# Performance work log

Measured on AMD Instinct MI355X. Metric: run time of the kernel, lower is better.

The kernel has to match this reference:

```python
import jax, jax.numpy as jnp
import numpy as np

S_INIT, S_FINAL = 512, 1024
LAYER_DIM, NEXT_DIM, DIM = 512, 512, 1024
BATCH = 32768


def setup_inputs() -> dict:
    rng = np.random.default_rng(0)
    # eigenvector block (trainable 'base') and its 0/1 mask
    base = np.zeros((DIM, DIM), dtype=np.float32)
    base[S_INIT:S_FINAL, S_INIT - LAYER_DIM:S_INIT] = rng.uniform(
        -0.2, 0.2, (NEXT_DIM, LAYER_DIM)).astype(np.float32)
    base_mask = np.zeros((DIM, DIM), dtype=np.float32)
    base_mask[S_INIT:S_FINAL, S_INIT - LAYER_DIM:S_INIT] = 1.0
    eye = np.eye(DIM, dtype=np.float32)
    # eigenvalue diagonal block; NOTE: trainable_diag_mask holds the *random values*
    # (not 0/1), exactly as in the original TF code.
    masks = np.zeros((DIM, DIM), dtype=np.float32)
    masks[S_INIT:S_FINAL, S_INIT:S_FINAL] = np.diag(
        rng.uniform(-1.8, 1.8, NEXT_DIM).astype(np.float32))
    untrainable_diag = eye - masks
    trainable_diag = masks.copy()
    trainable_diag_mask = masks.copy()
    # column masks selecting pass-through rows vs. activated block rows
    mask1 = np.ones((DIM, 1), dtype=np.float32)
    mask1[S_INIT:S_FINAL] = 0.0
    mask2 = np.zeros((DIM, 1), dtype=np.float32)
    mask2[S_INIT:S_FINAL] = 1.0

    key = jax.random.key(0)
    data = jax.random.normal(key, (BATCH, DIM), dtype=jnp.float32)
    return {
        "data": data,
        "base": jnp.asarray(base),
        "base_mask": jnp.asarray(base_mask),
        "eye": jnp.asarray(eye),
        "trainable_diag": jnp.asarray(trainable_diag),
        "trainable_diag_mask": jnp.asarray(trainable_diag_mask),
        "untrainable_diag": jnp.asarray(untrainable_diag),
        "mask1": jnp.asarray(mask1),
        "mask2": jnp.asarray(mask2),
    }


def reference(data, base, base_mask, eye, trainable_diag, trainable_diag_mask,
              untrainable_diag, mask1, mask2):
    # layer = masked base + I ; diag = masked trainable diag + (I - fixed diag)
    layer = base * base_mask + eye                                  # [D, D]
    diag = trainable_diag * trainable_diag_mask + untrainable_diag  # [D, D]
    x = jnp.matmul(2.0 * eye - layer, data.T)                       # [D, B]
    x = jnp.matmul(diag, x)                                         # [D, B]
    x = jnp.matmul(layer, x)                                        # [D, B]
    temp = jax.nn.relu(x)  # relu is elementwise; transpose pair cancels
    x = x * mask1 + temp * mask2                                    # [D, B]
    return x.T                                                      # [B, D]
```

## Files before the change

### kernel.cpp

```cpp
#include <hip/hip_runtime.h>


typedef float f32x4 __attribute__((ext_vector_type(4)));
typedef int   i32x4 __attribute__((ext_vector_type(4)));

#define DIMW   1024
#define HALFD  512
#define BM     128
#define BN     128
#define BK     32

__device__ __forceinline__ unsigned short f2bf(float x) {
    union { float f; unsigned int i; } c;
    c.f = x;
    unsigned int r = c.i + 0x7FFFu + ((c.i >> 16) & 1u);
    return (unsigned short)(r >> 16);
}
__device__ __forceinline__ unsigned int pack2(float a, float b) {
    return (unsigned int)f2bf(a) | ((unsigned int)f2bf(b) << 16);
}

__device__ __forceinline__ void mfma_16x16x32_bf16(f32x4& d, const i32x4& a, const i32x4& b) {
    asm volatile("v_mfma_f32_16x16x32_bf16 %0, %1, %2, %0"
                 : "+v"(d)
                 : "v"(a), "v"(b));
}
__device__ __forceinline__ void acc_fence(f32x4& d) {
    asm volatile("s_nop 7\n\ts_nop 7" : "+v"(d));
}

__global__ __launch_bounds__(256) void spectral_kernel(
    const float* __restrict__ data,
    const float* __restrict__ wsrc,
    const float* __restrict__ td,
    const float* __restrict__ tdm,
    const float* __restrict__ ud,
    float* __restrict__ out)
{
    __shared__ unsigned short As[BM * BK];
    __shared__ unsigned short Bs[BN * BK];
    __shared__ float dsh[BN];

    const int tid    = (int)threadIdx.x;
    const int lane   = tid & 63;
    const int wave   = tid >> 6;
    const int lane16 = lane & 15;
    const int quad   = lane >> 4;
    const int wm     = wave >> 1;
    const int wn     = wave & 1;
    const int rowBase = (int)blockIdx.x * BM;
    const int colBase = (int)blockIdx.y * BN;

    if (tid < BN) {
        int j = HALFD + colBase + tid;
        size_t fi = (size_t)j * DIMW + j;
        dsh[tid] = td[fi] * tdm[fi] + ud[fi];
    }

    {
        const float4* src = (const float4*)data;
        float4*       dst = (float4*)out;
        #pragma unroll
        for (int p = 0; p < 16; ++p) {
            int c  = p * 256 + tid;
            int r  = c >> 5;
            int cc = c & 31;
            size_t off = (size_t)(rowBase + r) * (DIMW / 4) + (colBase >> 2) + cc;
            dst[off] = src[off];
        }
    }

    f32x4 acc[4][4];
    #pragma unroll
    for (int mi = 0; mi < 4; ++mi)
        #pragma unroll
        for (int ni = 0; ni < 4; ++ni)
            acc[mi][ni] = (f32x4){0.f, 0.f, 0.f, 0.f};

    for (int k0 = 0; k0 < HALFD; k0 += BK) {
        float4 av[4], bv[4];
        #pragma unroll
        for (int p = 0; p < 4; ++p) {
            int c  = p * 256 + tid;
            int r  = c >> 3;
            int kc = (c & 7) * 4;
            av[p] = *(const float4*)(data + (size_t)(rowBase + r) * DIMW + k0 + kc);
            bv[p] = *(const float4*)(wsrc + (size_t)(HALFD + colBase + r) * DIMW + k0 + kc);
        }
        __syncthreads();
        #pragma unroll
        for (int p = 0; p < 4; ++p) {
            int c  = p * 256 + tid;
            int r  = c >> 3;
            int kc = (c & 7) * 4;
            uint2 ua, ub;
            ua.x = pack2(av[p].x, av[p].y);  ua.y = pack2(av[p].z, av[p].w);
            ub.x = pack2(bv[p].x, bv[p].y);  ub.y = pack2(bv[p].z, bv[p].w);
            *(uint2*)(As + r * BK + kc) = ua;
            *(uint2*)(Bs + r * BK + kc) = ub;
        }
        __syncthreads();

        i32x4 a[4], b[4];
        #pragma unroll
        for (int mi = 0; mi < 4; ++mi)
            a[mi] = *(const i32x4*)(As + (wm * 64 + mi * 16 + lane16) * BK + quad * 8);
        #pragma unroll
        for (int ni = 0; ni < 4; ++ni)
            b[ni] = *(const i32x4*)(Bs + (wn * 64 + ni * 16 + lane16) * BK + quad * 8);

        #pragma unroll
        for (int mi = 0; mi < 4; ++mi)
            #pragma unroll
            for (int ni = 0; ni < 4; ++ni)
                mfma_16x16x32_bf16(acc[mi][ni], a[mi], b[ni]);
    }

    #pragma unroll
    for (int mi = 0; mi < 4; ++mi)
        #pragma unroll
        for (int ni = 0; ni < 4; ++ni)
            acc_fence(acc[mi][ni]);

    #pragma unroll
    for (int mi = 0; mi < 4; ++mi) {
        int mBase = rowBase + wm * 64 + mi * 16 + quad * 4;
        #pragma unroll
        for (int ni = 0; ni < 4; ++ni) {
            int nloc = wn * 64 + ni * 16 + lane16;
            float dv = dsh[nloc];
            int col  = HALFD + colBase + nloc;
            #pragma unroll
            for (int r = 0; r < 4; ++r) {
                int row  = mBase + r;
                size_t gi = (size_t)row * DIMW + col;
                float u1 = data[gi];
                float v  = dv * u1 + (1.0f - dv) * acc[mi][ni][r];
                out[gi] = fmaxf(v, 0.0f);
            }
        }
    }
}

extern "C" void kernel_launch(void* const* d_in, const int* in_sizes, int n_in,
                              void* d_out, int out_size, void* d_ws, size_t ws_size,
                              hipStream_t stream) {
    const float* data = (const float*)d_in[0];
    const float* base = (const float*)d_in[1];
    const float* td   = (const float*)d_in[4];
    const float* tdm  = (const float*)d_in[5];
    const float* ud   = (const float*)d_in[6];
    float* out = (float*)d_out;

    dim3 grid(32768 / BM, HALFD / BN);
    dim3 block(256, 1, 1);
    spectral_kernel<<<grid, block, 0, stream>>>(data, base, td, tdm, ud, out);
}
```

Baseline: 302.4 us.

## Double-buffer LDS tiles with register prefetch, XOR-swizzle LDS, move passthrough copy to end

Splits the K loop into load, pack and compute stages. The next tile's global loads are issued before the MFMAs on the current tile, and two LDS buffers alternate between iterations. LDS addresses get an XOR swizzle to reduce bank conflicts on the 16-byte fragment reads. The pass-through copy of the first half of the columns moves after the epilogue, and launch bounds now request 3 blocks per SM, which may constrain register allocation. The cost is doubled LDS and held prefetch registers, with a possible risk of spills.

```diff
diff --git a/kernel.cpp b/kernel.cpp
--- a/kernel.cpp
+++ b/kernel.cpp
@@ -9,6 +9,7 @@
 #define BM     128
 #define BN     128
 #define BK     32
+#define NITER  16
 
 __device__ __forceinline__ unsigned short f2bf(float x) {
     union { float f; unsigned int i; } c;
@@ -29,7 +30,7 @@
     asm volatile("s_nop 7\n\ts_nop 7" : "+v"(d));
 }
 
-__global__ __launch_bounds__(256) void spectral_kernel(
+__global__ __launch_bounds__(256, 3) void spectral_kernel(
     const float* __restrict__ data,
     const float* __restrict__ wsrc,
     const float* __restrict__ td,
@@ -37,8 +38,8 @@
     const float* __restrict__ ud,
     float* __restrict__ out)
 {
-    __shared__ unsigned short As[BM * BK];
-    __shared__ unsigned short Bs[BN * BK];
+    __shared__ unsigned short As[2][BM * BK];
+    __shared__ unsigned short Bs[2][BN * BK];
     __shared__ float dsh[BN];
 
     const int tid    = (int)threadIdx.x;
@@ -57,19 +58,6 @@
         dsh[tid] = td[fi] * tdm[fi] + ud[fi];
     }
 
-    {
-        const float4* src = (const float4*)data;
-        float4*       dst = (float4*)out;
-        #pragma unroll
-        for (int p = 0; p < 16; ++p) {
-            int c  = p * 256 + tid;
-            int r  = c >> 5;
-            int cc = c & 31;
-            size_t off = (size_t)(rowBase + r) * (DIMW / 4) + (colBase >> 2) + cc;
-            dst[off] = src[off];
-        }
-    }
-
     f32x4 acc[4][4];
     #pragma unroll
     for (int mi = 0; mi < 4; ++mi)
@@ -77,8 +65,9 @@
         for (int ni = 0; ni < 4; ++ni)
             acc[mi][ni] = (f32x4){0.f, 0.f, 0.f, 0.f};
 
-    for (int k0 = 0; k0 < HALFD; k0 += BK) {
-        float4 av[4], bv[4];
+    float4 av[4], bv[4];
+
+    auto LOADT = [&](int k0) {
         #pragma unroll
         for (int p = 0; p < 4; ++p) {
             int c  = p * 256 + tid;
@@ -87,33 +76,54 @@
             av[p] = *(const float4*)(data + (size_t)(rowBase + r) * DIMW + k0 + kc);
             bv[p] = *(const float4*)(wsrc + (size_t)(HALFD + colBase + r) * DIMW + k0 + kc);
         }
-        __syncthreads();
+    };
+    auto PACKW = [&](int buf) {
         #pragma unroll
         for (int p = 0; p < 4; ++p) {
-            int c  = p * 256 + tid;
-            int r  = c >> 3;
-            int kc = (c & 7) * 4;
+            int c    = p * 256 + tid;
+            int r    = c >> 3;
+            int half = c & 7;
+            int idx = r * BK + ((((half >> 1) ^ ((r >> 1) & 3)) << 3)) + (half & 1) * 4;
             uint2 ua, ub;
             ua.x = pack2(av[p].x, av[p].y);  ua.y = pack2(av[p].z, av[p].w);
             ub.x = pack2(bv[p].x, bv[p].y);  ub.y = pack2(bv[p].z, bv[p].w);
-            *(uint2*)(As + r * BK + kc) = ua;
-            *(uint2*)(Bs + r * BK + kc) = ub;
+            *(uint2*)(&As[buf][idx]) = ua;
+            *(uint2*)(&Bs[buf][idx]) = ub;
         }
-        __syncthreads();
+    };
+
+    LOADT(0);
+    PACKW(0);
+    __syncthreads();
+
+    for (int it = 0; it < NITER; ++it) {
+        const int cur = it & 1;
+
+        if (it + 1 < NITER) LOADT((it + 1) * BK);
 
         i32x4 a[4], b[4];
         #pragma unroll
-        for (int mi = 0; mi < 4; ++mi)
-            a[mi] = *(const i32x4*)(As + (wm * 64 + mi * 16 + lane16) * BK + quad * 8);
+        for (int mi = 0; mi < 4; ++mi) {
+            int R = wm * 64 + mi * 16 + lane16;
+            a[mi] = *(const i32x4*)(&As[cur][R * BK + ((quad ^ ((R >> 1) & 3)) << 3)]);
+        }
         #pragma unroll
-        for (int ni = 0; ni < 4; ++ni)
-            b[ni] = *(const i32x4*)(Bs + (wn * 64 + ni * 16 + lane16) * BK + quad * 8);
+        for (int ni = 0; ni < 4; ++ni) {
+            int R = wn * 64 + ni * 16 + lane16;
+            b[ni] = *(const i32x4*)(&Bs[cur][R * BK + ((quad ^ ((R >> 1) & 3)) << 3)]);
+        }
 
         #pragma unroll
         for (int mi = 0; mi < 4; ++mi)
             #pragma unroll
             for (int ni = 0; ni < 4; ++ni)
                 mfma_16x16x32_bf16(acc[mi][ni], a[mi], b[ni]);
+
+        __syncthreads();
+        if (it + 1 < NITER) {
+            PACKW(cur ^ 1);
+            __syncthreads();
+        }
     }
 
     #pragma unroll
@@ -140,6 +150,19 @@
             }
         }
     }
+
+    {
+        const float4* src = (const float4*)data;
+        float4*       dst = (float4*)out;
+        #pragma unroll
+        for (int p = 0; p < 16; ++p) {
+            int c  = p * 256 + tid;
+            int r  = c >> 5;
+            int cc = c & 31;
+            size_t off = (size_t)(rowBase + r) * (DIMW / 4) + (colBase >> 2) + cc;
+            dst[off] = src[off];
+        }
+    }
 }
 
 extern "C" void kernel_launch(void* const* d_in, const int* in_sizes, int n_in,
```

Result: no change. 302.2 us (-0.1%).

## Keep full-K weight panel in LDS and stream A directly into registers

Applied to the files above, without the earlier changes.

Each block now holds a 64-column bf16 weight panel covering the full K range in swizzled LDS, loaded once at the start. A fragments are read from global memory straight into registers with double buffering, so the per-K-step syncthreads and the LDS staging of A are gone. Tile N shrinks to 64 with launch bounds set to 2 blocks per CU, and the pass-through copy moves after the epilogue. The cost is 64KB of LDS per block and uncoalesced 32-byte strided A loads, and the data tile is re-read by twice as many blocks.

```diff
diff --git a/kernel.cpp b/kernel.cpp
--- a/kernel.cpp
+++ b/kernel.cpp
@@ -3,12 +3,13 @@
 
 typedef float f32x4 __attribute__((ext_vector_type(4)));
 typedef int   i32x4 __attribute__((ext_vector_type(4)));
+typedef unsigned int u32x4 __attribute__((ext_vector_type(4)));
 
 #define DIMW   1024
 #define HALFD  512
 #define BM     128
-#define BN     128
-#define BK     32
+#define BN     64
+#define NITER  16
 
 __device__ __forceinline__ unsigned short f2bf(float x) {
     union { float f; unsigned int i; } c;
@@ -29,7 +30,11 @@
     asm volatile("s_nop 7\n\ts_nop 7" : "+v"(d));
 }
 
-__global__ __launch_bounds__(256) void spectral_kernel(
+__device__ __forceinline__ int bs_addr(int col, int k) {
+    return (col * 1024 + k * 2) ^ ((((col & 7) ^ ((k >> 7) & 3))) << 4);
+}
+
+__global__ __launch_bounds__(256, 2) void spectral_kernel(
     const float* __restrict__ data,
     const float* __restrict__ wsrc,
     const float* __restrict__ td,
@@ -37,9 +42,7 @@
     const float* __restrict__ ud,
     float* __restrict__ out)
 {
-    __shared__ unsigned short As[BM * BK];
-    __shared__ unsigned short Bs[BN * BK];
-    __shared__ float dsh[BN];
+    __shared__ unsigned short Bs[BN * HALFD];
 
     const int tid    = (int)threadIdx.x;
     const int lane   = tid & 63;
@@ -51,93 +54,109 @@
     const int rowBase = (int)blockIdx.x * BM;
     const int colBase = (int)blockIdx.y * BN;
 
-    if (tid < BN) {
-        int j = HALFD + colBase + tid;
-        size_t fi = (size_t)j * DIMW + j;
-        dsh[tid] = td[fi] * tdm[fi] + ud[fi];
+    {
+        const int cw = tid >> 2;
+        const int ks = (tid & 3) * 128;
+        const float* wr = wsrc + (size_t)(HALFD + colBase + cw) * DIMW + ks;
+        #pragma unroll
+        for (int g = 0; g < 16; ++g) {
+            const int k = ks + g * 8;
+            float4 f0 = *(const float4*)(wr + g * 8);
+            float4 f1 = *(const float4*)(wr + g * 8 + 4);
+            u32x4 u;
+            u[0] = pack2(f0.x, f0.y);  u[1] = pack2(f0.z, f0.w);
+            u[2] = pack2(f1.x, f1.y);  u[3] = pack2(f1.z, f1.w);
+            *(u32x4*)((char*)Bs + bs_addr(cw, k)) = u;
+        }
+    }
+    __syncthreads();
+
+    f32x4 acc[4][2];
+    #pragma unroll
+    for (int mi = 0; mi < 4; ++mi)
+        #pragma unroll
+        for (int ni = 0; ni < 2; ++ni)
+            acc[mi][ni] = (f32x4){0.f, 0.f, 0.f, 0.f};
+
+    const float* abase = data + (size_t)(rowBase + wm * 64 + lane16) * DIMW + quad * 8;
+
+    float4 x0[4], x1[4], y0[4], y1[4];
+    auto LDA = [&](int k0, float4 (&q0)[4], float4 (&q1)[4]) {
+        #pragma unroll
+        for (int mi = 0; mi < 4; ++mi) {
+            const float* p = abase + (size_t)(mi * 16) * DIMW + k0;
+            q0[mi] = *(const float4*)p;
+            q1[mi] = *(const float4*)(p + 4);
+        }
+    };
+    auto STEP = [&](int it, float4 (&q0)[4], float4 (&q1)[4]) {
+        i32x4 a[4];
+        #pragma unroll
+        for (int mi = 0; mi < 4; ++mi) {
+            i32x4 t;
+            t[0] = (int)pack2(q0[mi].x, q0[mi].y);
+            t[1] = (int)pack2(q0[mi].z, q0[mi].w);
+            t[2] = (int)pack2(q1[mi].x, q1[mi].y);
+            t[3] = (int)pack2(q1[mi].z, q1[mi].w);
+            a[mi] = t;
+        }
+        i32x4 b[2];
+        #pragma unroll
+        for (int ni = 0; ni < 2; ++ni) {
+            const int col = wn * 32 + ni * 16 + lane16;
+            b[ni] = *(const i32x4*)((const char*)Bs + bs_addr(col, it * 32 + quad * 8));
+        }
+        #pragma unroll
+        for (int mi = 0; mi < 4; ++mi)
+            #pragma unroll
+            for (int ni = 0; ni < 2; ++ni)
+                mfma_16x16x32_bf16(acc[mi][ni], a[mi], b[ni]);
+    };
+
+    LDA(0, x0, x1);
+    #pragma unroll
+    for (int it = 0; it < NITER; it += 2) {
+        LDA((it + 1) * 32, y0, y1);
+        STEP(it, x0, x1);
+        if (it + 2 < NITER) LDA((it + 2) * 32, x0, x1);
+        STEP(it + 1, y0, y1);
+    }
+
+    #pragma unroll
+    for (int mi = 0; mi < 4; ++mi)
+        #pragma unroll
+        for (int ni = 0; ni < 2; ++ni)
+            acc_fence(acc[mi][ni]);
+
+    #pragma unroll
+    for (int ni = 0; ni < 2; ++ni) {
+        const int nloc = wn * 32 + ni * 16 + lane16;
+        const int j  = HALFD + colBase + nloc;
+        const size_t fi = (size_t)j * DIMW + j;
+        const float dv = td[fi] * tdm[fi] + ud[fi];
+        #pragma unroll
+        for (int mi = 0; mi < 4; ++mi) {
+            const int mBase = rowBase + wm * 64 + mi * 16 + quad * 4;
+            #pragma unroll
+            for (int r = 0; r < 4; ++r) {
+                const size_t gi = (size_t)(mBase + r) * DIMW + j;
+                const float u1 = data[gi];
+                const float v  = dv * u1 + (1.0f - dv) * acc[mi][ni][r];
+                out[gi] = fmaxf(v, 0.0f);
+            }
+        }
     }
 
     {
         const float4* src = (const float4*)data;
         float4*       dst = (float4*)out;
         #pragma unroll
-        for (int p = 0; p < 16; ++p) {
+        for (int p = 0; p < 8; ++p) {
             int c  = p * 256 + tid;
-            int r  = c >> 5;
-            int cc = c & 31;
+            int r  = c >> 4;
+            int cc = c & 15;
             size_t off = (size_t)(rowBase + r) * (DIMW / 4) + (colBase >> 2) + cc;
             dst[off] = src[off];
-        }
-    }
-
-    f32x4 acc[4][4];
-    #pragma unroll
-    for (int mi = 0; mi < 4; ++mi)
-        #pragma unroll
-        for (int ni = 0; ni < 4; ++ni)
-            acc[mi][ni] = (f32x4){0.f, 0.f, 0.f, 0.f};
-
-    for (int k0 = 0; k0 < HALFD; k0 += BK) {
-        float4 av[4], bv[4];
-        #pragma unroll
-        for (int p = 0; p < 4; ++p) {
-            int c  = p * 256 + tid;
-            int r  = c >> 3;
-            int kc = (c & 7) * 4;
-            av[p] = *(const float4*)(data + (size_t)(rowBase + r) * DIMW + k0 + kc);
-            bv[p] = *(const float4*)(wsrc + (size_t)(HALFD + colBase + r) * DIMW + k0 + kc);
-        }
-        __syncthreads();
-        #pragma unroll
-        for (int p = 0; p < 4; ++p) {
-            int c  = p * 256 + tid;
-            int r  = c >> 3;
-            int kc = (c & 7) * 4;
-            uint2 ua, ub;
-            ua.x = pack2(av[p].x, av[p].y);  ua.y = pack2(av[p].z, av[p].w);
-            ub.x = pack2(bv[p].x, bv[p].y);  ub.y = pack2(bv[p].z, bv[p].w);
-            *(uint2*)(As + r * BK + kc) = ua;
-            *(uint2*)(Bs + r * BK + kc) = ub;
-        }
-        __syncthreads();
-
-        i32x4 a[4], b[4];
-        #pragma unroll
-        for (int mi = 0; mi < 4; ++mi)
-            a[mi] = *(const i32x4*)(As + (wm * 64 + mi * 16 + lane16) * BK + quad * 8);
-        #pragma unroll
-        for (int ni = 0; ni < 4; ++ni)
-            b[ni] = *(const i32x4*)(Bs + (wn * 64 + ni * 16 + lane16) * BK + quad * 8);
-
-        #pragma unroll
-        for (int mi = 0; mi < 4; ++mi)
-            #pragma unroll
-            for (int ni = 0; ni < 4; ++ni)
-                mfma_16x16x32_bf16(acc[mi][ni], a[mi], b[ni]);
-    }
-
-    #pragma unroll
-    for (int mi = 0; mi < 4; ++mi)
-        #pragma unroll
-        for (int ni = 0; ni < 4; ++ni)
-            acc_fence(acc[mi][ni]);
-
-    #pragma unroll
-    for (int mi = 0; mi < 4; ++mi) {
-        int mBase = rowBase + wm * 64 + mi * 16 + quad * 4;
-        #pragma unroll
-        for (int ni = 0; ni < 4; ++ni) {
-            int nloc = wn * 64 + ni * 16 + lane16;
-            float dv = dsh[nloc];
-            int col  = HALFD + colBase + nloc;
-            #pragma unroll
-            for (int r = 0; r < 4; ++r) {
-                int row  = mBase + r;
-                size_t gi = (size_t)row * DIMW + col;
-                float u1 = data[gi];
-                float v  = dv * u1 + (1.0f - dv) * acc[mi][ni][r];
-                out[gi] = fmaxf(v, 0.0f);
-            }
         }
     }
 }
```

Result: slower. 389.8 us (+28.9%).

## Stage full-K data rows in LDS once and stream weights from registers

Applied to the files above, without the earlier changes.

Each block now owns 64 batch rows across all 512 output columns. It loads the row's full 512-wide K slice of data into padded LDS once as bf16, while also performing the pass-through copy. Weight fragments are read directly from global memory into registers with double buffering, so the per-K-step LDS staging and barriers go away, along with the repeated reads of data across column tiles. The cost is that every block rereads the entire 512x512 weight block from global or L2, and LDS use per block grows to about 66KB.

```diff
diff --git a/kernel.cpp b/kernel.cpp
--- a/kernel.cpp
+++ b/kernel.cpp
@@ -6,9 +6,9 @@
 
 #define DIMW   1024
 #define HALFD  512
-#define BM     128
-#define BN     128
-#define BK     32
+#define BM     64
+#define LDAP   520
+#define NITER  16
 
 __device__ __forceinline__ unsigned short f2bf(float x) {
     union { float f; unsigned int i; } c;
@@ -29,7 +29,7 @@
     asm volatile("s_nop 7\n\ts_nop 7" : "+v"(d));
 }
 
-__global__ __launch_bounds__(256) void spectral_kernel(
+__global__ __launch_bounds__(512, 4) void spectral_kernel(
     const float* __restrict__ data,
     const float* __restrict__ wsrc,
     const float* __restrict__ td,
@@ -37,38 +37,48 @@
     const float* __restrict__ ud,
     float* __restrict__ out)
 {
-    __shared__ unsigned short As[BM * BK];
-    __shared__ unsigned short Bs[BN * BK];
-    __shared__ float dsh[BN];
+    __shared__ unsigned short As[BM * LDAP];
 
     const int tid    = (int)threadIdx.x;
     const int lane   = tid & 63;
-    const int wave   = tid >> 6;
+    const int wn     = tid >> 6;
     const int lane16 = lane & 15;
     const int quad   = lane >> 4;
-    const int wm     = wave >> 1;
-    const int wn     = wave & 1;
     const int rowBase = (int)blockIdx.x * BM;
-    const int colBase = (int)blockIdx.y * BN;
 
-    if (tid < BN) {
-        int j = HALFD + colBase + tid;
-        size_t fi = (size_t)j * DIMW + j;
-        dsh[tid] = td[fi] * tdm[fi] + ud[fi];
+    #pragma unroll
+    for (int p = 0; p < 16; ++p) {
+        int c  = p * 512 + tid;
+        int r  = c >> 7;
+        int cc = c & 127;
+        size_t off = (size_t)(rowBase + r) * DIMW + cc * 4;
+        float4 v = *(const float4*)(data + off);
+        *(float4*)(out + off) = v;
+        uint2 uu;
+        uu.x = pack2(v.x, v.y);
+        uu.y = pack2(v.z, v.w);
+        *(uint2*)(As + r * LDAP + cc * 4) = uu;
     }
 
-    {
-        const float4* src = (const float4*)data;
-        float4*       dst = (float4*)out;
+    i32x4 b0[4], b1[4];
+
+    auto LDW = [&](int it, i32x4 (&b)[4]) {
         #pragma unroll
-        for (int p = 0; p < 16; ++p) {
-            int c  = p * 256 + tid;
-            int r  = c >> 5;
-            int cc = c & 31;
-            size_t off = (size_t)(rowBase + r) * (DIMW / 4) + (colBase >> 2) + cc;
-            dst[off] = src[off];
+        for (int ni = 0; ni < 4; ++ni) {
+            int col = wn * 64 + ni * 16 + lane16;
+            const float* p = wsrc + (size_t)(HALFD + col) * DIMW + it * 32 + quad * 8;
+            float4 f0 = *(const float4*)p;
+            float4 f1 = *(const float4*)(p + 4);
+            i32x4 t;
+            t[0] = (int)pack2(f0.x, f0.y);  t[1] = (int)pack2(f0.z, f0.w);
+            t[2] = (int)pack2(f1.x, f1.y);  t[3] = (int)pack2(f1.z, f1.w);
+            b[ni] = t;
         }
-    }
+    };
+
+    LDW(0, b0);
+    LDW(1, b1);
+    __syncthreads();
 
     f32x4 acc[4][4];
     #pragma unroll
@@ -77,43 +87,24 @@
         for (int ni = 0; ni < 4; ++ni)
             acc[mi][ni] = (f32x4){0.f, 0.f, 0.f, 0.f};
 
-    for (int k0 = 0; k0 < HALFD; k0 += BK) {
-        float4 av[4], bv[4];
-        #pragma unroll
-        for (int p = 0; p < 4; ++p) {
-            int c  = p * 256 + tid;
-            int r  = c >> 3;
-            int kc = (c & 7) * 4;
-            av[p] = *(const float4*)(data + (size_t)(rowBase + r) * DIMW + k0 + kc);
-            bv[p] = *(const float4*)(wsrc + (size_t)(HALFD + colBase + r) * DIMW + k0 + kc);
-        }
-        __syncthreads();
-        #pragma unroll
-        for (int p = 0; p < 4; ++p) {
-            int c  = p * 256 + tid;
-            int r  = c >> 3;
-            int kc = (c & 7) * 4;
-            uint2 ua, ub;
-            ua.x = pack2(av[p].x, av[p].y);  ua.y = pack2(av[p].z, av[p].w);
-            ub.x = pack2(bv[p].x, bv[p].y);  ub.y = pack2(bv[p].z, bv[p].w);
-            *(uint2*)(As + r * BK + kc) = ua;
-            *(uint2*)(Bs + r * BK + kc) = ub;
-        }
-        __syncthreads();
-
-        i32x4 a[4], b[4];
+    auto STEP = [&](int it, i32x4 (&b)[4]) {
+        i32x4 a[4];
         #pragma unroll
         for (int mi = 0; mi < 4; ++mi)
-            a[mi] = *(const i32x4*)(As + (wm * 64 + mi * 16 + lane16) * BK + quad * 8);
-        #pragma unroll
-        for (int ni = 0; ni < 4; ++ni)
-            b[ni] = *(const i32x4*)(Bs + (wn * 64 + ni * 16 + lane16) * BK + quad * 8);
-
+            a[mi] = *(const i32x4*)(As + (mi * 16 + lane16) * LDAP + it * 32 + quad * 8);
         #pragma unroll
         for (int mi = 0; mi < 4; ++mi)
             #pragma unroll
             for (int ni = 0; ni < 4; ++ni)
                 mfma_16x16x32_bf16(acc[mi][ni], a[mi], b[ni]);
+    };
+
+    #pragma unroll
+    for (int it = 0; it < NITER; it += 2) {
+        STEP(it, b0);
+        if (it + 2 < NITER) LDW(it + 2, b0);
+        STEP(it + 1, b1);
+        if (it + 3 < NITER) LDW(it + 3, b1);
     }
 
     #pragma unroll
@@ -123,19 +114,19 @@
             acc_fence(acc[mi][ni]);
 
     #pragma unroll
-    for (int mi = 0; mi < 4; ++mi) {
-        int mBase = rowBase + wm * 64 + mi * 16 + quad * 4;
+    for (int ni = 0; ni < 4; ++ni) {
+        const int nloc = wn * 64 + ni * 16 + lane16;
+        const int j  = HALFD + nloc;
+        const size_t fi = (size_t)j * DIMW + j;
+        const float dv = td[fi] * tdm[fi] + ud[fi];
         #pragma unroll
-        for (int ni = 0; ni < 4; ++ni) {
-            int nloc = wn * 64 + ni * 16 + lane16;
-            float dv = dsh[nloc];
-            int col  = HALFD + colBase + nloc;
+        for (int mi = 0; mi < 4; ++mi) {
+            const int mBase = rowBase + mi * 16 + quad * 4;
             #pragma unroll
             for (int r = 0; r < 4; ++r) {
-                int row  = mBase + r;
-                size_t gi = (size_t)row * DIMW + col;
-                float u1 = data[gi];
-                float v  = dv * u1 + (1.0f - dv) * acc[mi][ni][r];
+                const size_t gi = (size_t)(mBase + r) * DIMW + j;
+                const float u1 = data[gi];
+                const float v  = dv * u1 + (1.0f - dv) * acc[mi][ni][r];
                 out[gi] = fmaxf(v, 0.0f);
             }
         }
@@ -152,7 +143,7 @@
     const float* ud   = (const float*)d_in[6];
     float* out = (float*)d_out;
 
-    dim3 grid(32768 / BM, HALFD / BN);
-    dim3 block(256, 1, 1);
+    dim3 block(512, 1, 1);
+    dim3 grid(32768 / BM, 1, 1);
     spectral_kernel<<<grid, block, 0, stream>>>(data, base, td, tdm, ud, out);
 }
```

Result: slower. 367.4 us (+21.5%).
